# Kernel optimization log

Measured on AMD Instinct MI355X. Metric: run time of the kernel, lower is better.

## Reference

```python
import jax, jax.numpy as jnp
import numpy as np


def setup_inputs() -> dict:
    key = jax.random.key(0)
    ks = jax.random.split(key, 5)
    B, C, H, W = 4, 64, 64, 64
    C8 = C // 8
    return {
        "x_opt": jax.random.normal(ks[0], (B, C, H, W), jnp.float32),
        "x_sar": jax.random.normal(ks[1], (B, C, H, W), jnp.float32),
        "wq": jax.random.normal(ks[2], (C8, C), jnp.float32) * 0.05,
        "bq": jnp.zeros((C8,), jnp.float32),
        "wk": jax.random.normal(ks[3], (C8, C), jnp.float32) * 0.05,
        "bk": jnp.zeros((C8,), jnp.float32),
        "wv": jax.random.normal(ks[4], (C, C), jnp.float32) * 0.05,
        "bv": jnp.zeros((C,), jnp.float32),
        "gamma": jnp.zeros((1,), jnp.float32),
    }


def reference(x_opt, x_sar, wq, bq, wk, bk, wv, bv, gamma):
    b, c, h, w = x_opt.shape
    n = h * w
    xo = x_opt.reshape(b, c, n)  # [b, c, N]
    xs = x_sar.reshape(b, c, n)
    # 1x1 convs == channel matmuls
    q = jnp.einsum('oc,bcn->bon', wq, xo) + bq[None, :, None]  # [b, c//8, N]
    k = jnp.einsum('oc,bcn->bon', wk, xs) + bk[None, :, None]  # [b, c//8, N]
    v = jnp.einsum('oc,bcn->bon', wv, xs) + bv[None, :, None]  # [b, c, N]
    # attn[b, n, m] = softmax_m( q[:, :, n] . k[:, :, m] )  -- NO 1/sqrt(d) scaling
    scores = jnp.einsum('bdn,bdm->bnm', q, k)  # [b, N, N]
    attn = jax.nn.softmax(scores, axis=-1)
    # out[b, c, n] = sum_m v[b, c, m] * attn[b, n, m]
    out = jnp.einsum('bcm,bnm->bcn', v, attn).reshape(b, c, h, w)
    return gamma[0] * out + x_opt
```

## Files before the change

### kernel.cpp

```cpp
#include <hip/hip_runtime.h>
#include <hip/hip_bf16.h>
#include <stdint.h>

#define NDIM 4096
#define CDIM 64
#define NSPLIT 8
#define SPAN (NDIM / NSPLIT)
#define NQ4 (SPAN / 32)
#define LOG2E 1.44269504088896f

typedef float f32x4 __attribute__((ext_vector_type(4)));
typedef float f32x16 __attribute__((ext_vector_type(16)));
typedef short bf16x8 __attribute__((ext_vector_type(8)));
union U4B { uint4 u; bf16x8 b; };

static __device__ __forceinline__ uint32_t cvtpk(float lo, float hi) {
  uint32_t r;
  asm("v_cvt_pk_bf16_f32 %0, %1, %2" : "=v"(r) : "v"(lo), "v"(hi));
  return r;
}
static __device__ __forceinline__ uint16_t f2bf(float f) {
  uint32_t r;
  asm("v_cvt_pk_bf16_f32 %0, %1, %1" : "=v"(r) : "v"(f));
  return (uint16_t)r;
}
static __device__ __forceinline__ float fexp2(float x) {
  return __builtin_amdgcn_exp2f(x);
}

__global__ __launch_bounds__(256) void proj_kernel(
    const float* __restrict__ x_opt, const float* __restrict__ x_sar,
    const float* __restrict__ wq, const float* __restrict__ bq,
    const float* __restrict__ wk, const float* __restrict__ bk,
    const float* __restrict__ wvp, const float* __restrict__ bv,
    uint16_t* __restrict__ qf, uint16_t* __restrict__ kfp,
    uint16_t* __restrict__ vf2)
{
  const int tid = threadIdx.x;
  const int w = tid >> 6;
  const int l = tid & 63;
  const int x = l & 31;
  const int hi = l >> 5;

  const int id = blockIdx.x;
  const int b = id >> 7;
  const int n0 = (id & 127) * 32;
  const size_t xbase = (size_t)b * CDIM * NDIM;

  const float* xsrc = (w == 2) ? x_opt : x_sar;
  bf16x8 xB[4];
#pragma unroll
  for (int kc = 0; kc < 4; kc++) {
    float sv[8];
#pragma unroll
    for (int j = 0; j < 8; j++)
      sv[j] = xsrc[xbase + (size_t)(kc * 16 + hi * 8 + j) * NDIM + n0 + x];
    U4B us;
    us.u = make_uint4(cvtpk(sv[0], sv[1]), cvtpk(sv[2], sv[3]),
                      cvtpk(sv[4], sv[5]), cvtpk(sv[6], sv[7]));
    xB[kc] = us.b;
  }

  bf16x8 aF[4];
#pragma unroll
  for (int kc = 0; kc < 4; kc++) {
    U4B ua;
    ua.u = make_uint4(0u, 0u, 0u, 0u);
    if (w < 2) {
      const float* wr = wvp + (w * 32 + x) * 64 + kc * 16 + hi * 8;
      float4 wa = ((const float4*)wr)[0];
      float4 wb = ((const float4*)wr)[1];
      ua.u = make_uint4(cvtpk(wa.x, wa.y), cvtpk(wa.z, wa.w),
                        cvtpk(wb.x, wb.y), cvtpk(wb.z, wb.w));
    } else if (x < 8) {
      const float* wr = ((w == 2) ? wq : wk) + x * 64 + kc * 16 + hi * 8;
      float4 wa = ((const float4*)wr)[0];
      float4 wb = ((const float4*)wr)[1];
      ua.u = make_uint4(cvtpk(wa.x, wa.y), cvtpk(wa.z, wa.w),
                        cvtpk(wb.x, wb.y), cvtpk(wb.z, wb.w));
    }
    aF[kc] = ua.b;
  }

  const f32x16 z16 = {0.f,0.f,0.f,0.f, 0.f,0.f,0.f,0.f,
                      0.f,0.f,0.f,0.f, 0.f,0.f,0.f,0.f};
  f32x16 acc = z16;
#pragma unroll
  for (int kc = 0; kc < 4; kc++)
    acc = __builtin_amdgcn_mfma_f32_32x32x16_bf16(aF[kc], xB[kc], acc, 0, 0, 0);

  if (w < 2) {
    const size_t kbbase = (size_t)b * 256 + (n0 >> 4) + (x >> 4);
    const int kk = x & 15;
#pragma unroll
    for (int r = 0; r < 16; r++) {
      const int row = w * 32 + (r & 3) + 8 * (r >> 2) + 4 * hi;
      vf2[(kbbase * 64 + row) * 16 + kk] = f2bf(acc[r] + bv[row]);
    }
  } else if (w == 2) {
    float gv[4];
#pragma unroll
    for (int r = 0; r < 4; r++) gv[r] = (acc[r] + bq[4 * hi + r]) * LOG2E;
    const size_t nrow = ((size_t)b * NDIM + n0 + x) * 16;
    uint2 st;
    st.x = cvtpk(gv[0], gv[1]); st.y = cvtpk(gv[2], gv[3]);
    *(uint2*)(qf + nrow + hi * 4) = st;
    if (hi == 0) {
      const uint4 z4 = make_uint4(0u, 0u, 0u, 0u);
      *(uint4*)(qf + nrow + 8) = z4;
    }
  } else {
    float gv[4];
#pragma unroll
    for (int r = 0; r < 4; r++) gv[r] = acc[r] + bk[4 * hi + r];
    uint2 st;
    st.x = cvtpk(gv[0], gv[1]); st.y = cvtpk(gv[2], gv[3]);
    *(uint2*)(kfp + ((size_t)b * NDIM + n0 + x) * 8 + hi * 4) = st;
  }
}

__global__ __launch_bounds__(256, 4) void attn_kernel(
    const uint16_t* __restrict__ qf, const uint16_t* __restrict__ kfp,
    const uint16_t* __restrict__ vf2,
    uint16_t* __restrict__ po2, float* __restrict__ ls)
{
  const int tid = threadIdx.x;
  const int w = tid >> 6;
  const int l = tid & 63;
  const int x = l & 31;
  const int hi = l >> 5;

  const int id = blockIdx.x;
  const int sp = id & 7;
  const int qb = (id >> 3) & 31;
  const int b = id >> 8;

  const int n0 = qb * 128;
  const int qrow = n0 + w * 32 + x;
  const int skew = qb & 15;

  U4B qfr;
  qfr.u = *(const uint4*)(qf + ((size_t)b * NDIM + qrow) * 16 + hi * 8);

  const uint16_t* ksb = kfp + ((size_t)b * NDIM + sp * SPAN) * 8;
  const uint16_t* vsb = vf2 + (((size_t)b * 256 + sp * 32) * 64) * 16;
  const int klane = x * 8;
  const int vlane = x * 16 + hi * 8;

  const f32x16 z16 = {0.f,0.f,0.f,0.f, 0.f,0.f,0.f,0.f,
                      0.f,0.f,0.f,0.f, 0.f,0.f,0.f,0.f};
  f32x16 oacc0 = z16, oacc1 = z16;
  float lacc[4] = {0.f, 0.f, 0.f, 0.f};

  uint4 kA, vA0, vA1, vA2, vA3;
  {
    const int e0 = skew;
    kA  = *(const uint4*)(ksb + e0 * 256 + klane);
    vA0 = *(const uint4*)(vsb + e0 * 2048 + vlane);
    vA1 = *(const uint4*)(vsb + e0 * 2048 + 512 + vlane);
    vA2 = *(const uint4*)(vsb + e0 * 2048 + 1024 + vlane);
    vA3 = *(const uint4*)(vsb + e0 * 2048 + 1536 + vlane);
  }

#pragma unroll
  for (int gq = 0; gq < NQ4; gq++) {
    const int e1 = (gq + 1 + skew) & 15;
    uint4 kn   = *(const uint4*)(ksb + e1 * 256 + klane);
    uint4 vn0  = *(const uint4*)(vsb + e1 * 2048 + vlane);
    uint4 vn1  = *(const uint4*)(vsb + e1 * 2048 + 512 + vlane);
    uint4 vn2  = *(const uint4*)(vsb + e1 * 2048 + 1024 + vlane);
    uint4 vn3  = *(const uint4*)(vsb + e1 * 2048 + 1536 + vlane);

    U4B ka; ka.u = kA;
    f32x16 s = __builtin_amdgcn_mfma_f32_32x32x16_bf16(ka.b, qfr.b, z16, 0, 0, 0);

    uint32_t W[8];
#pragma unroll
    for (int j = 0; j < 8; j++) {
      const float p0 = fexp2(s[2 * j]);
      const float p1 = fexp2(s[2 * j + 1]);
      W[j] = cvtpk(p0, p1);
      lacc[j & 3] += p0 + p1;
    }

    __builtin_amdgcn_s_setprio(1);
    {
      uint32_t a0 = W[0], b0 = W[2], a1 = W[1], b1 = W[3];
      asm("v_permlane32_swap_b32 %0, %1" : "+v"(a0), "+v"(b0));
      asm("v_permlane32_swap_b32 %0, %1" : "+v"(a1), "+v"(b1));
      U4B pf, va, vb;
      pf.u = make_uint4(a0, a1, b0, b1);
      va.u = vA0; vb.u = vA1;
      oacc0 = __builtin_amdgcn_mfma_f32_32x32x16_bf16(va.b, pf.b, oacc0, 0, 0, 0);
      oacc1 = __builtin_amdgcn_mfma_f32_32x32x16_bf16(vb.b, pf.b, oacc1, 0, 0, 0);
    }
    {
      uint32_t a0 = W[4], b0 = W[6], a1 = W[5], b1 = W[7];
      asm("v_permlane32_swap_b32 %0, %1" : "+v"(a0), "+v"(b0));
      asm("v_permlane32_swap_b32 %0, %1" : "+v"(a1), "+v"(b1));
      U4B pf, va, vb;
      pf.u = make_uint4(a0, a1, b0, b1);
      va.u = vA2; vb.u = vA3;
      oacc0 = __builtin_amdgcn_mfma_f32_32x32x16_bf16(va.b, pf.b, oacc0, 0, 0, 0);
      oacc1 = __builtin_amdgcn_mfma_f32_32x32x16_bf16(vb.b, pf.b, oacc1, 0, 0, 0);
    }
    __builtin_amdgcn_s_setprio(0);

    kA = kn; vA0 = vn0; vA1 = vn1; vA2 = vn2; vA3 = vn3;
  }

  {
    uint16_t* pb = po2 + ((size_t)(sp * 256 + b * 64 + hi * 4)) * NDIM + qrow;
#pragma unroll
    for (int r = 0; r < 16; r++) {
      const size_t off = (size_t)((r & 3) + 8 * (r >> 2)) * NDIM;
      pb[off] = f2bf(oacc0[r]);
      pb[off + (size_t)32 * NDIM] = f2bf(oacc1[r]);
    }
  }
  float ltot = (lacc[0] + lacc[1]) + (lacc[2] + lacc[3]);
  ltot += __shfl_xor(ltot, 32);
  if (hi == 0)
    ls[((size_t)sp * 4 + b) * NDIM + qrow] = ltot;
}

__global__ __launch_bounds__(256) void merge_kernel(
    const uint16_t* __restrict__ po2, const float* __restrict__ ls,
    const float* __restrict__ x_opt, const float* __restrict__ gamma,
    float* __restrict__ out)
{
  const int idx = blockIdx.x * 256 + threadIdx.x;
  const int n8 = (idx & 511) << 3;
  const int row = idx >> 9;
  const int b = row >> 6;

  float acc[8] = {0.f, 0.f, 0.f, 0.f, 0.f, 0.f, 0.f, 0.f};
  f32x4 ws0 = {0.f, 0.f, 0.f, 0.f};
  f32x4 ws1 = {0.f, 0.f, 0.f, 0.f};
#pragma unroll
  for (int s = 0; s < NSPLIT; s++) {
    const uint4 pv = *(const uint4*)(po2 + ((size_t)s * 256 + row) * NDIM + n8);
    const uint32_t* pw = (const uint32_t*)&pv;
#pragma unroll
    for (int j = 0; j < 4; j++) {
      acc[j * 2 + 0] += __uint_as_float(pw[j] << 16);
      acc[j * 2 + 1] += __uint_as_float(pw[j] & 0xFFFF0000u);
    }
    const float* lp = ls + ((size_t)s * 4 + b) * NDIM + n8;
    ws0 += *(const f32x4*)(lp);
    ws1 += *(const f32x4*)(lp + 4);
  }
  const float gm = gamma[0];
  const float* xp = x_opt + (size_t)row * NDIM + n8;
  float* op = out + (size_t)row * NDIM + n8;
  float4 x0 = ((const float4*)xp)[0];
  float4 x1 = ((const float4*)xp)[1];
  float4 o0, o1;
  o0.x = gm * acc[0] / ws0[0] + x0.x;
  o0.y = gm * acc[1] / ws0[1] + x0.y;
  o0.z = gm * acc[2] / ws0[2] + x0.z;
  o0.w = gm * acc[3] / ws0[3] + x0.w;
  o1.x = gm * acc[4] / ws1[0] + x1.x;
  o1.y = gm * acc[5] / ws1[1] + x1.y;
  o1.z = gm * acc[6] / ws1[2] + x1.z;
  o1.w = gm * acc[7] / ws1[3] + x1.w;
  ((float4*)op)[0] = o0;
  ((float4*)op)[1] = o1;
}

extern "C" void kernel_launch(void* const* d_in, const int* in_sizes, int n_in,
                              void* d_out, int out_size, void* d_ws, size_t ws_size,
                              hipStream_t stream) {
  const float* x_opt = (const float*)d_in[0];
  const float* x_sar = (const float*)d_in[1];
  const float* wq    = (const float*)d_in[2];
  const float* bq    = (const float*)d_in[3];
  const float* wk    = (const float*)d_in[4];
  const float* bk    = (const float*)d_in[5];
  const float* wvp   = (const float*)d_in[6];
  const float* bv    = (const float*)d_in[7];
  const float* gamma = (const float*)d_in[8];
  float* outp = (float*)d_out;

  uint16_t* qf  = (uint16_t*)d_ws;
  uint16_t* kfp = (uint16_t*)((char*)d_ws + 524288);
  uint16_t* vf2 = (uint16_t*)((char*)d_ws + 1048576);
  uint16_t* po2 = (uint16_t*)((char*)d_ws + 3145728);
  float* lsp    = (float*)((char*)d_ws + 19922944);

  proj_kernel<<<512, 256, 0, stream>>>(x_opt, x_sar, wq, bq, wk, bk, wvp, bv,
                                       qf, kfp, vf2);
  attn_kernel<<<1024, 256, 0, stream>>>(qf, kfp, vf2, po2, lsp);
  merge_kernel<<<512, 256, 0, stream>>>(po2, lsp, x_opt, gamma, outp);
}
```

Baseline: 36.63 us.

## Remap block IDs to group shared K/V spans per XCD and drop skew

Changes how block IDs map to (batch, query block, split), so that blocks dispatched round-robin to the same XCD share a batch and key/value span. The goal is better L2 reuse of K/V on each chiplet. The per-block skew of the starting key chunk is removed, so blocks on a span now walk it in the same order. This could concentrate simultaneous reads on the same addresses, which may help cache hits or cause channel contention.

```diff
diff --git a/kernel.cpp b/kernel.cpp
--- a/kernel.cpp
+++ b/kernel.cpp
@@ -131,13 +131,14 @@
   const int hi = l >> 5;
 
   const int id = blockIdx.x;
-  const int sp = id & 7;
-  const int qb = (id >> 3) & 31;
-  const int b = id >> 8;
+  const int x8 = id & 7;
+  const int j  = id >> 3;
+  const int b  = x8 & 3;
+  const int sp = ((x8 >> 2) << 2) | ((j >> 2) & 3);
+  const int qb = (j & 3) | (((j >> 4) & 7) << 2);
 
   const int n0 = qb * 128;
   const int qrow = n0 + w * 32 + x;
-  const int skew = qb & 15;
 
   U4B qfr;
   qfr.u = *(const uint4*)(qf + ((size_t)b * NDIM + qrow) * 16 + hi * 8);
@@ -152,35 +153,31 @@
   f32x16 oacc0 = z16, oacc1 = z16;
   float lacc[4] = {0.f, 0.f, 0.f, 0.f};
 
-  uint4 kA, vA0, vA1, vA2, vA3;
-  {
-    const int e0 = skew;
-    kA  = *(const uint4*)(ksb + e0 * 256 + klane);
-    vA0 = *(const uint4*)(vsb + e0 * 2048 + vlane);
-    vA1 = *(const uint4*)(vsb + e0 * 2048 + 512 + vlane);
-    vA2 = *(const uint4*)(vsb + e0 * 2048 + 1024 + vlane);
-    vA3 = *(const uint4*)(vsb + e0 * 2048 + 1536 + vlane);
-  }
+  uint4 kA  = *(const uint4*)(ksb + klane);
+  uint4 vA0 = *(const uint4*)(vsb + vlane);
+  uint4 vA1 = *(const uint4*)(vsb + 512 + vlane);
+  uint4 vA2 = *(const uint4*)(vsb + 1024 + vlane);
+  uint4 vA3 = *(const uint4*)(vsb + 1536 + vlane);
 
 #pragma unroll
   for (int gq = 0; gq < NQ4; gq++) {
-    const int e1 = (gq + 1 + skew) & 15;
-    uint4 kn   = *(const uint4*)(ksb + e1 * 256 + klane);
-    uint4 vn0  = *(const uint4*)(vsb + e1 * 2048 + vlane);
-    uint4 vn1  = *(const uint4*)(vsb + e1 * 2048 + 512 + vlane);
-    uint4 vn2  = *(const uint4*)(vsb + e1 * 2048 + 1024 + vlane);
-    uint4 vn3  = *(const uint4*)(vsb + e1 * 2048 + 1536 + vlane);
+    const int e1 = (gq + 1) & 15;
+    uint4 kn  = *(const uint4*)(ksb + e1 * 256 + klane);
+    uint4 vn0 = *(const uint4*)(vsb + e1 * 2048 + vlane);
+    uint4 vn1 = *(const uint4*)(vsb + e1 * 2048 + 512 + vlane);
+    uint4 vn2 = *(const uint4*)(vsb + e1 * 2048 + 1024 + vlane);
+    uint4 vn3 = *(const uint4*)(vsb + e1 * 2048 + 1536 + vlane);
 
     U4B ka; ka.u = kA;
     f32x16 s = __builtin_amdgcn_mfma_f32_32x32x16_bf16(ka.b, qfr.b, z16, 0, 0, 0);
 
     uint32_t W[8];
 #pragma unroll
-    for (int j = 0; j < 8; j++) {
-      const float p0 = fexp2(s[2 * j]);
-      const float p1 = fexp2(s[2 * j + 1]);
-      W[j] = cvtpk(p0, p1);
-      lacc[j & 3] += p0 + p1;
+    for (int jj = 0; jj < 8; jj++) {
+      const float p0 = fexp2(s[2 * jj]);
+      const float p1 = fexp2(s[2 * jj + 1]);
+      W[jj] = cvtpk(p0, p1);
+      lacc[jj & 3] += p0 + p1;
     }
 
     __builtin_amdgcn_s_setprio(1);
```

Result: no change. 36.75 us (+0.3%).
